# Optimization experiments

Measured on AMD Instinct MI355X. Metric: run time of the kernel, lower is better.

## Reference

```python
import jax, jax.numpy as jnp
import numpy as np

NUM_HEADS = 16
LN_EPS = 1e-5


def setup_inputs() -> dict:
    key = jax.random.key(0)
    ks = jax.random.split(key, 7)
    B, S, D = 4, 1024, 1024
    s_in = 1.0 / np.sqrt(D)
    return {
        "x": jax.random.normal(ks[0], (B, S, D), dtype=jnp.float32),
        # PyTorch MHA packed in-projection: [3D, D] weight, [3D] bias
        "w_qkv": jax.random.uniform(ks[1], (3 * D, D), dtype=jnp.float32, minval=-s_in, maxval=s_in),
        "b_qkv": jnp.zeros((3 * D,), dtype=jnp.float32),
        "w_out": jax.random.uniform(ks[2], (D, D), dtype=jnp.float32, minval=-s_in, maxval=s_in),
        "b_out": jnp.zeros((D,), dtype=jnp.float32),
        "ln_w": jnp.ones((D,), dtype=jnp.float32),
        "ln_b": jnp.zeros((D,), dtype=jnp.float32),
    }


def _layernorm(x, w, b):
    m = jnp.mean(x, axis=-1, keepdims=True)
    v = jnp.var(x, axis=-1, keepdims=True)
    return (x - m) * jax.lax.rsqrt(v + LN_EPS) * w + b


def reference(x, w_qkv, b_qkv, w_out, b_out, ln_w, ln_b):
    B, S, D = x.shape
    H = NUM_HEADS
    hd = D // H
    # packed QKV projection (torch: F.linear(x, w_qkv, b_qkv) then chunk)
    qkv = x @ w_qkv.T + b_qkv                      # [B, S, 3D]
    q, k, v = jnp.split(qkv, 3, axis=-1)
    q = q.reshape(B, S, H, hd).transpose(0, 2, 1, 3) * (hd ** -0.5)  # [B,H,S,hd]
    k = k.reshape(B, S, H, hd).transpose(0, 2, 1, 3)
    v = v.reshape(B, S, H, hd).transpose(0, 2, 1, 3)
    scores = jnp.einsum('bhqd,bhkd->bhqk', q, k)   # [B,H,S,S]
    attn = jax.nn.softmax(scores, axis=-1)
    ctx = jnp.einsum('bhqk,bhkd->bhqd', attn, v)   # [B,H,S,hd]
    ctx = ctx.transpose(0, 2, 1, 3).reshape(B, S, D)
    attn_out = ctx @ w_out.T + b_out
    # torch returns head-averaged weights (average_attn_weights=True)
    attn_weights = attn.mean(axis=1)               # [B,S,S]
    # dropout rate 0.0 -> identity; residual + LayerNorm
    y = _layernorm(x + attn_out, ln_w, ln_b)
    return y, attn_weights
```

## Files before the change

### kernel.cpp

```cpp
#include <hip/hip_runtime.h>
#include <cstdint>

typedef __bf16 bf16;
typedef __bf16 bf16x8 __attribute__((ext_vector_type(8)));
typedef __bf16 bf16x4 __attribute__((ext_vector_type(4)));
typedef float  f32x4  __attribute__((ext_vector_type(4)));

#define MFMA_BF16(a, b, c) __builtin_amdgcn_mfma_f32_16x16x32_bf16(a, b, c, 0, 0, 0)

#define WAITCNT_VM(n) asm volatile("s_waitcnt vmcnt(" #n ")" ::: "memory")
#define CFENCE()      asm volatile("" ::: "memory")

__device__ __forceinline__ void async_load16(const void* g, void* l) {
    __builtin_amdgcn_global_load_lds(
        (__attribute__((address_space(1))) uint32_t*)(uintptr_t)g,
        (__attribute__((address_space(3))) uint32_t*)(uint32_t)(uintptr_t)l,
        16, 0, 0);
}

__global__ void cvt_kernel(const float* __restrict__ src, bf16* __restrict__ dst, int n4) {
    int i = blockIdx.x * blockDim.x + threadIdx.x;
    if (i < n4) {
        float4 v = ((const float4*)src)[i];
        bf16x4 o;
        o[0] = (bf16)v.x; o[1] = (bf16)v.y; o[2] = (bf16)v.z; o[3] = (bf16)v.w;
        ((bf16x4*)dst)[i] = o;
    }
}

__global__ __launch_bounds__(256) void gemm_qkv_kernel(
    const bf16* __restrict__ A, const bf16* __restrict__ W,
    const float* __restrict__ bias,
    bf16* __restrict__ Qb, bf16* __restrict__ Kb, bf16* __restrict__ Vt)
{
    const int Kd = 1024;
    __shared__ bf16 sA[3][128 * 32];
    __shared__ bf16 sB[3][128 * 32];
    int tid = threadIdx.x, lane = tid & 63, wid = tid >> 6;
    int flat = blockIdx.y * 24 + blockIdx.x;
    int orig = (flat & 7) * 96 + (flat >> 3);
    int m0 = (orig / 24) * 128, n0 = (orig % 24) * 128;
    int srow = wid * 32 + (lane >> 2);
    int pchunk = lane & 3;
    int jchunk = pchunk ^ ((lane >> 3) & 3);
    const bf16* Ag = A + (size_t)(m0 + srow) * Kd + jchunk * 8;
    const bf16* Wg = W + (size_t)(n0 + srow) * Kd + jchunk * 8;
    int soff = srow * 32 + pchunk * 8;
    int wm = (wid & 1) * 64, wn = (wid >> 1) * 64;
    int lcol = lane & 15, quad = lane >> 4;
    int ckey = (lcol >> 1) & 3;
    f32x4 acc[4][4] = {};
#define STG_Q(buf, k0_) do { \
        async_load16(Ag + (k0_), &sA[buf][soff]); \
        async_load16(Ag + (k0_) + 16 * Kd, &sA[buf][soff + 512]); \
        async_load16(Wg + (k0_), &sB[buf][soff]); \
        async_load16(Wg + (k0_) + 16 * Kd, &sB[buf][soff + 512]); \
    } while (0)
    STG_Q(0, 0);
    STG_Q(1, 32);
    STG_Q(2, 64);
    int cur = 0;
    for (int it = 0; it < 32; ++it) {
        if (it < 30)      { WAITCNT_VM(8); }
        else if (it == 30){ WAITCNT_VM(4); }
        else              { WAITCNT_VM(0); }
        __builtin_amdgcn_s_barrier();
        CFENCE();
        const bf16* cA = sA[cur];
        const bf16* cB = sB[cur];
        bf16x8 af[4], bfr[4];
#pragma unroll
        for (int i = 0; i < 4; i++)
            af[i] = *(const bf16x8*)&cA[(wm + i * 16 + lcol) * 32 + (quad ^ ckey) * 8];
#pragma unroll
        for (int i = 0; i < 4; i++)
            bfr[i] = *(const bf16x8*)&cB[(wn + i * 16 + lcol) * 32 + (quad ^ ckey) * 8];
#pragma unroll
        for (int i = 0; i < 4; i++)
#pragma unroll
            for (int j = 0; j < 4; j++)
                acc[i][j] = MFMA_BF16(af[i], bfr[j], acc[i][j]);
        CFENCE();
        __builtin_amdgcn_s_barrier();
        if (it + 3 < 32) STG_Q(cur, (it + 3) * 32);
        cur = (cur == 2) ? 0 : cur + 1;
    }
#undef STG_Q
#pragma unroll
    for (int j = 0; j < 4; j++) {
        int n = n0 + wn + j * 16 + lcol;
        float bv = bias[n];
        int part = n >> 10, d = n & 1023, h = d >> 6, dd = d & 63;
#pragma unroll
        for (int i = 0; i < 4; i++) {
            int mb = m0 + wm + i * 16 + quad * 4;
            int b = mb >> 10, s = mb & 1023;
            if (part == 2) {
                bf16x4 v4;
#pragma unroll
                for (int r = 0; r < 4; r++) v4[r] = (bf16)(acc[i][j][r] + bv);
                *(bf16x4*)&Vt[(size_t)((b * 16 + h) * 64 + dd) * 1024 + s] = v4;
            } else {
                float scv = (part == 0) ? 0.125f : 1.0f;
                bf16* dst = (part == 0 ? Qb : Kb) + (size_t)((b * 16 + h) * 1024 + s) * 64 + dd;
#pragma unroll
                for (int r = 0; r < 4; r++) dst[(size_t)r * 64] = (bf16)((acc[i][j][r] + bv) * scv);
            }
        }
    }
}

__global__ __launch_bounds__(256) void gemm_out_kernel(
    const bf16* __restrict__ A, const bf16* __restrict__ W,
    const float* __restrict__ bias, float* __restrict__ out)
{
    const int Kd = 1024;
    __shared__ bf16 sA[3][64 * 32];
    __shared__ bf16 sB[3][128 * 32];
    int tid = threadIdx.x, lane = tid & 63, wid = tid >> 6;
    int m0 = blockIdx.y * 64, n0 = blockIdx.x * 128;
    int ra = tid >> 2;
    int pchunk = tid & 3;
    int jchunk = pchunk ^ ((tid >> 3) & 3);
    const bf16* Ag = A + (size_t)(m0 + ra) * Kd + jchunk * 8;
    const bf16* Wg = W + (size_t)(n0 + ra) * Kd + jchunk * 8;
    int aoff = ra * 32 + pchunk * 8;
    int wm = (wid & 1) * 32, wn = (wid >> 1) * 64;
    int lcol = lane & 15, quad = lane >> 4;
    int ckey = (lcol >> 1) & 3;
    f32x4 acc[2][4] = {};
#define STG_O(buf, k0_) do { \
        async_load16(Ag + (k0_), &sA[buf][aoff]); \
        async_load16(Wg + (k0_), &sB[buf][aoff]); \
        async_load16(Wg + (k0_) + 64 * Kd, &sB[buf][aoff + 64 * 32]); \
    } while (0)
    STG_O(0, 0);
    STG_O(1, 32);
    STG_O(2, 64);
    int cur = 0;
    for (int it = 0; it < 32; ++it) {
        if (it < 30)      { WAITCNT_VM(6); }
        else if (it == 30){ WAITCNT_VM(3); }
        else              { WAITCNT_VM(0); }
        __builtin_amdgcn_s_barrier();
        CFENCE();
        const bf16* cA = sA[cur];
        const bf16* cB = sB[cur];
        bf16x8 af[2], bfr[4];
#pragma unroll
        for (int i = 0; i < 2; i++)
            af[i] = *(const bf16x8*)&cA[(wm + i * 16 + lcol) * 32 + (quad ^ ckey) * 8];
#pragma unroll
        for (int j = 0; j < 4; j++)
            bfr[j] = *(const bf16x8*)&cB[(wn + j * 16 + lcol) * 32 + (quad ^ ckey) * 8];
#pragma unroll
        for (int i = 0; i < 2; i++)
#pragma unroll
            for (int j = 0; j < 4; j++)
                acc[i][j] = MFMA_BF16(af[i], bfr[j], acc[i][j]);
        CFENCE();
        __builtin_amdgcn_s_barrier();
        if (it + 3 < 32) STG_O(cur, (it + 3) * 32);
        cur = (cur == 2) ? 0 : cur + 1;
    }
#undef STG_O
#pragma unroll
    for (int j = 0; j < 4; j++) {
        int n = n0 + wn + j * 16 + lcol;
        float bv = bias[n];
#pragma unroll
        for (int i = 0; i < 2; i++) {
            int m = m0 + wm + i * 16 + quad * 4;
#pragma unroll
            for (int r = 0; r < 4; r++) out[(size_t)(m + r) * 1024 + n] = acc[i][j][r] + bv;
        }
    }
}

__global__ __launch_bounds__(512) void flash_kernel(
    const bf16* __restrict__ Qb, const bf16* __restrict__ Kb, const bf16* __restrict__ Vt,
    bf16* __restrict__ ctx, float* __restrict__ ml)
{
    __shared__ bf16 sK[2][64 * 64];
    __shared__ bf16 sV[2][64 * 64];
    __shared__ bf16 pt[8][16 * 64];
    int tid = threadIdx.x, lane = tid & 63, wid = tid >> 6;
    int bx = blockIdx.x;
    int orig = (bx & 7) * 64 + (bx >> 3);
    int qt = orig & 7;
    int h = (orig >> 3) & 15;
    int b = orig >> 7;
    int lcol = lane & 15, quad = lane >> 4;
    size_t base = (size_t)(b * 16 + h) * 65536;

    int q0 = qt * 128 + wid * 16;
    const bf16* qp = Qb + base + (size_t)(q0 + lcol) * 64 + quad * 8;
    bf16x8 a0 = *(const bf16x8*)qp;
    bf16x8 a1 = *(const bf16x8*)(qp + 32);

    char* wpt = (char*)&pt[wid][0];
    int sr = tid >> 3;
    int pp = tid & 7;
    int jj = pp ^ (sr & 7);
    int sw = lcol & 7;

#define STAGE_KV(buf, kt_) do { \
        async_load16(Kb + base + (size_t)((kt_) * 64 + sr) * 64 + jj * 8, &sK[buf][sr * 64 + pp * 8]); \
        async_load16(Vt + base + (size_t)sr * 1024 + (kt_) * 64 + jj * 8, &sV[buf][sr * 64 + pp * 8]); \
    } while (0)

    float l_[4] = {0.f, 0.f, 0.f, 0.f};
    f32x4 o[4] = {};

    STAGE_KV(0, 0);
    int cur = 0;
    for (int kt = 0; kt < 16; kt++) {
        __syncthreads();
        if (kt < 15) STAGE_KV(cur ^ 1, kt + 1);
        const bf16* sKc = &sK[cur][0];
        const bf16* sVc = &sV[cur][0];
#pragma unroll
        for (int nt = 0; nt < 4; nt++) {
            int ck = quad ^ sw;
            bf16x8 bk0 = *(const bf16x8*)&sKc[(nt * 16 + lcol) * 64 + ck * 8];
            bf16x8 bk1 = *(const bf16x8*)&sKc[(nt * 16 + lcol) * 64 + (ck ^ 4) * 8];
            f32x4 s = {};
            s = MFMA_BF16(a0, bk0, s);
            s = MFMA_BF16(a1, bk1, s);
#pragma unroll
            for (int rr = 0; rr < 4; rr++) {
                float p = __expf(s[rr]);
                l_[rr] += p;
                int row = quad * 4 + rr;
                *(bf16*)(wpt + row * 128 + ((nt * 32 + lcol * 2) ^ ((row & 7) << 4))) = (bf16)p;
            }
        }
#pragma unroll
        for (int kf = 0; kf < 2; kf++) {
            bf16x8 pa = *(const bf16x8*)(wpt + lcol * 128 + (((kf * 4 + quad) ^ sw) << 4));
#pragma unroll
            for (int dt = 0; dt < 4; dt++) {
                bf16x8 vb = *(const bf16x8*)&sVc[(dt * 16 + lcol) * 64 + ((kf * 4 + quad) ^ sw) * 8];
                o[dt] = MFMA_BF16(pa, vb, o[dt]);
            }
        }
        cur ^= 1;
    }
#undef STAGE_KV
#pragma unroll
    for (int mk = 1; mk < 16; mk <<= 1)
#pragma unroll
        for (int rr = 0; rr < 4; rr++) l_[rr] += __shfl_xor(l_[rr], mk, 64);
#pragma unroll
    for (int rr = 0; rr < 4; rr++) {
        float inv = 1.f / l_[rr];
        int qg = q0 + quad * 4 + rr;
#pragma unroll
        for (int dt = 0; dt < 4; dt++)
            ctx[(size_t)(b * 1024 + qg) * 1024 + h * 64 + dt * 16 + lcol] = (bf16)(o[dt][rr] * inv);
        if (lcol == 0)
            ml[(size_t)(b * 16 + h) * 1024 + qg] = l_[rr];
    }
}

__global__ __launch_bounds__(512) void aw_kernel(
    const bf16* __restrict__ Qb, const bf16* __restrict__ Kb,
    const float* __restrict__ ml, float* __restrict__ aw)
{
    __shared__ bf16 sK[2][64 * 64];
    int tid = threadIdx.x, lane = tid & 63, wid = tid >> 6;
    int bx = blockIdx.x;
    int orig = (bx & 7) * 64 + (bx >> 3);
    int kt = orig & 15;
    int qt = (orig >> 4) & 7;
    int b = orig >> 7;
    int lcol = lane & 15, quad = lane >> 4;
    int q0 = qt * 128 + wid * 16;
    int kbase = kt * 64;
    int sw = lcol & 7;
    int sr = tid >> 3, pp = tid & 7, jj = pp ^ (sr & 7);

#define STAGE_K(buf, hh) \
        async_load16(Kb + (size_t)(b * 16 + (hh)) * 65536 + (size_t)(kbase + sr) * 64 + jj * 8, \
                     &sK[buf][sr * 64 + pp * 8])

    float acc[16];
#pragma unroll
    for (int i = 0; i < 16; i++) acc[i] = 0.f;

    bf16x8 a0c, a1c, a0n, a1n;
    float4 mvC, mvN;
    {
        const bf16* qp = Qb + (size_t)(b * 16) * 65536 + (size_t)(q0 + lcol) * 64 + quad * 8;
        a0c = *(const bf16x8*)qp;
        a1c = *(const bf16x8*)(qp + 32);
        mvC = *(const float4*)(ml + (size_t)(b * 16) * 1024 + q0 + quad * 4);
    }
    STAGE_K(0, 0);
    int cur = 0;
    for (int h = 0; h < 16; h++) {
        __syncthreads();
        if (h < 15) {
            STAGE_K(cur ^ 1, h + 1);
            const bf16* qp = Qb + (size_t)(b * 16 + h + 1) * 65536 + (size_t)(q0 + lcol) * 64 + quad * 8;
            a0n = *(const bf16x8*)qp;
            a1n = *(const bf16x8*)(qp + 32);
            mvN = *(const float4*)(ml + (size_t)(b * 16 + h + 1) * 1024 + q0 + quad * 4);
        }
        float scale[4] = {0.0625f / mvC.x, 0.0625f / mvC.y, 0.0625f / mvC.z, 0.0625f / mvC.w};
#pragma unroll
        for (int nt = 0; nt < 4; nt++) {
            int ck = quad ^ sw;
            bf16x8 bk0 = *(const bf16x8*)&sK[cur][(nt * 16 + lcol) * 64 + ck * 8];
            bf16x8 bk1 = *(const bf16x8*)&sK[cur][(nt * 16 + lcol) * 64 + (ck ^ 4) * 8];
            f32x4 s = {};
            s = MFMA_BF16(a0c, bk0, s);
            s = MFMA_BF16(a1c, bk1, s);
#pragma unroll
            for (int rr = 0; rr < 4; rr++)
                acc[nt * 4 + rr] += __expf(s[rr]) * scale[rr];
        }
        if (h < 15) { a0c = a0n; a1c = a1n; mvC = mvN; }
        cur ^= 1;
    }
#undef STAGE_K
#pragma unroll
    for (int nt = 0; nt < 4; nt++)
#pragma unroll
        for (int rr = 0; rr < 4; rr++)
            aw[(size_t)(b * 1024 + q0 + quad * 4 + rr) * 1024 + kbase + nt * 16 + lcol] = acc[nt * 4 + rr];
}

__global__ __launch_bounds__(256) void ln_kernel(
    const float* __restrict__ x, const float* __restrict__ ao,
    const float* __restrict__ w, const float* __restrict__ bsh,
    float* __restrict__ y)
{
    int row = blockIdx.x, tid = threadIdx.x;
    float4 xv = ((const float4*)(x + (size_t)row * 1024))[tid];
    float4 av = ((const float4*)(ao + (size_t)row * 1024))[tid];
    float4 v = {xv.x + av.x, xv.y + av.y, xv.z + av.z, xv.w + av.w};
    float s = v.x + v.y + v.z + v.w;
    float ss = v.x * v.x + v.y * v.y + v.z * v.z + v.w * v.w;
#pragma unroll
    for (int off = 32; off; off >>= 1) { s += __shfl_down(s, off); ss += __shfl_down(ss, off); }
    __shared__ float rs[4], rss[4];
    int lane = tid & 63, wid = tid >> 6;
    if (lane == 0) { rs[wid] = s; rss[wid] = ss; }
    __syncthreads();
    s = rs[0] + rs[1] + rs[2] + rs[3];
    ss = rss[0] + rss[1] + rss[2] + rss[3];
    float mean = s * (1.f / 1024.f);
    float var = ss * (1.f / 1024.f) - mean * mean;
    float inv = rsqrtf(var + 1e-5f);
    float4 wv = ((const float4*)w)[tid];
    float4 bv = ((const float4*)bsh)[tid];
    float4 o;
    o.x = (v.x - mean) * inv * wv.x + bv.x;
    o.y = (v.y - mean) * inv * wv.y + bv.y;
    o.z = (v.z - mean) * inv * wv.z + bv.z;
    o.w = (v.w - mean) * inv * wv.w + bv.w;
    ((float4*)y)[row * 256 + tid] = o;
}

extern "C" void kernel_launch(void* const* d_in, const int* in_sizes, int n_in,
                              void* d_out, int out_size, void* d_ws, size_t ws_size,
                              hipStream_t stream) {
    const float* x     = (const float*)d_in[0];
    const float* w_qkv = (const float*)d_in[1];
    const float* b_qkv = (const float*)d_in[2];
    const float* w_out = (const float*)d_in[3];
    const float* b_out = (const float*)d_in[4];
    const float* ln_w  = (const float*)d_in[5];
    const float* ln_b  = (const float*)d_in[6];

    char* ws = (char*)d_ws;
    bf16*   Qb    = (bf16*)(ws);
    bf16*   Kb    = (bf16*)(ws + (8ull  << 20));
    bf16*   Vt    = (bf16*)(ws + (16ull << 20));
    bf16*   ctx   = (bf16*)(ws + (24ull << 20));
    float*  ml    = (float*)(ws + (32ull << 20));
    bf16*   x_bf  = (bf16*)(ws + (33ull << 20));
    bf16*   wq_bf = (bf16*)(ws + (41ull << 20));
    bf16*   wo_bf = (bf16*)(ws + (16ull << 20));
    float*  ao    = (float*)(ws);

    float* y_out  = (float*)d_out;
    float* aw_out = y_out + 4ull * 1024 * 1024;

    cvt_kernel<<<4096, 256, 0, stream>>>(x, x_bf, 1048576);
    cvt_kernel<<<3072, 256, 0, stream>>>(w_qkv, wq_bf, 786432);
    gemm_qkv_kernel<<<dim3(24, 32), 256, 0, stream>>>(x_bf, wq_bf, b_qkv, Qb, Kb, Vt);
    flash_kernel<<<512, 512, 0, stream>>>(Qb, Kb, Vt, ctx, ml);
    aw_kernel<<<512, 512, 0, stream>>>(Qb, Kb, ml, aw_out);
    cvt_kernel<<<1024, 256, 0, stream>>>(w_out, wo_bf, 262144);
    gemm_out_kernel<<<dim3(8, 64), 256, 0, stream>>>(ctx, wo_bf, b_out, ao);
    ln_kernel<<<4096, 256, 0, stream>>>(x, ao, ln_w, ln_b, y_out);
}
```

Before: 208.9 us.

## Stage GEMM and attention epilogues through LDS and merge conversion launches

The QKV GEMM epilogue now writes each output tile into shared memory and then emits coalesced 16-byte stores to Q, K and the transposed V, replacing scattered 2-byte and 8-byte global stores. The flash kernel likewise stages its context output through its per-warp LDS scratch so it can write 16-byte vectors. The two input conversion kernels become one launch, and the w_out conversion is folded into extra blocks of the attention-weights kernel. This cuts uncoalesced store traffic and launch count, at the cost of extra LDS traffic and a barrier in the epilogues.

```diff
diff --git a/kernel.cpp b/kernel.cpp
--- a/kernel.cpp
+++ b/kernel.cpp
@@ -18,14 +18,16 @@
         16, 0, 0);
 }
 
-__global__ void cvt_kernel(const float* __restrict__ src, bf16* __restrict__ dst, int n4) {
+__global__ void cvt3_kernel(const float* __restrict__ s0, bf16* __restrict__ d0, int n0,
+                            const float* __restrict__ s1, bf16* __restrict__ d1, int n1) {
     int i = blockIdx.x * blockDim.x + threadIdx.x;
-    if (i < n4) {
-        float4 v = ((const float4*)src)[i];
-        bf16x4 o;
-        o[0] = (bf16)v.x; o[1] = (bf16)v.y; o[2] = (bf16)v.z; o[3] = (bf16)v.w;
-        ((bf16x4*)dst)[i] = o;
-    }
+    const float* s; bf16* d; int j = i;
+    if (j < n0) { s = s0; d = d0; }
+    else { j -= n0; if (j >= n1) return; s = s1; d = d1; }
+    float4 v = ((const float4*)s)[j];
+    bf16x4 o;
+    o[0] = (bf16)v.x; o[1] = (bf16)v.y; o[2] = (bf16)v.z; o[3] = (bf16)v.w;
+    ((bf16x4*)d)[j] = o;
 }
 
 __global__ __launch_bounds__(256) void gemm_qkv_kernel(
@@ -34,8 +36,9 @@
     bf16* __restrict__ Qb, bf16* __restrict__ Kb, bf16* __restrict__ Vt)
 {
     const int Kd = 1024;
-    __shared__ bf16 sA[3][128 * 32];
-    __shared__ bf16 sB[3][128 * 32];
+    __shared__ __attribute__((aligned(16))) bf16 smem[6 * 128 * 32];
+    bf16* const sA0 = smem;
+    bf16* const sB0 = smem + 3 * 4096;
     int tid = threadIdx.x, lane = tid & 63, wid = tid >> 6;
     int flat = blockIdx.y * 24 + blockIdx.x;
     int orig = (flat & 7) * 96 + (flat >> 3);
@@ -51,10 +54,10 @@
     int ckey = (lcol >> 1) & 3;
     f32x4 acc[4][4] = {};
 #define STG_Q(buf, k0_) do { \
-        async_load16(Ag + (k0_), &sA[buf][soff]); \
-        async_load16(Ag + (k0_) + 16 * Kd, &sA[buf][soff + 512]); \
-        async_load16(Wg + (k0_), &sB[buf][soff]); \
-        async_load16(Wg + (k0_) + 16 * Kd, &sB[buf][soff + 512]); \
+        async_load16(Ag + (k0_), sA0 + (buf) * 4096 + soff); \
+        async_load16(Ag + (k0_) + 16 * Kd, sA0 + (buf) * 4096 + soff + 512); \
+        async_load16(Wg + (k0_), sB0 + (buf) * 4096 + soff); \
+        async_load16(Wg + (k0_) + 16 * Kd, sB0 + (buf) * 4096 + soff + 512); \
     } while (0)
     STG_Q(0, 0);
     STG_Q(1, 32);
@@ -66,8 +69,8 @@
         else              { WAITCNT_VM(0); }
         __builtin_amdgcn_s_barrier();
         CFENCE();
-        const bf16* cA = sA[cur];
-        const bf16* cB = sB[cur];
+        const bf16* cA = sA0 + cur * 4096;
+        const bf16* cB = sB0 + cur * 4096;
         bf16x8 af[4], bfr[4];
 #pragma unroll
         for (int i = 0; i < 4; i++)
@@ -86,26 +89,49 @@
         cur = (cur == 2) ? 0 : cur + 1;
     }
 #undef STG_Q
-#pragma unroll
-    for (int j = 0; j < 4; j++) {
-        int n = n0 + wn + j * 16 + lcol;
-        float bv = bias[n];
-        int part = n >> 10, d = n & 1023, h = d >> 6, dd = d & 63;
-#pragma unroll
-        for (int i = 0; i < 4; i++) {
-            int mb = m0 + wm + i * 16 + quad * 4;
-            int b = mb >> 10, s = mb & 1023;
-            if (part == 2) {
-                bf16x4 v4;
-#pragma unroll
-                for (int r = 0; r < 4; r++) v4[r] = (bf16)(acc[i][j][r] + bv);
-                *(bf16x4*)&Vt[(size_t)((b * 16 + h) * 64 + dd) * 1024 + s] = v4;
-            } else {
-                float scv = (part == 0) ? 0.125f : 1.0f;
-                bf16* dst = (part == 0 ? Qb : Kb) + (size_t)((b * 16 + h) * 1024 + s) * 64 + dd;
-#pragma unroll
-                for (int r = 0; r < 4; r++) dst[(size_t)r * 64] = (bf16)((acc[i][j][r] + bv) * scv);
-            }
+    const int LP = 136;
+    bf16* sE = smem;
+    int part = n0 >> 10;
+    int h0 = (n0 & 1023) >> 6;
+    int b = m0 >> 10, s0 = m0 & 1023;
+    if (part == 2) {
+#pragma unroll
+        for (int j = 0; j < 4; j++) {
+            float bv = bias[n0 + wn + j * 16 + lcol];
+#pragma unroll
+            for (int i = 0; i < 4; i++)
+#pragma unroll
+                for (int r = 0; r < 4; r++)
+                    sE[(wn + j * 16 + lcol) * LP + (wm + i * 16 + quad * 4 + r)] = (bf16)(acc[i][j][r] + bv);
+        }
+        __syncthreads();
+#pragma unroll
+        for (int p = 0; p < 8; p++) {
+            int c = p * 256 + tid;
+            int nl = c >> 4, mc = (c & 15) * 8;
+            int dd = nl & 63, h = h0 + (nl >> 6);
+            *(bf16x8*)&Vt[(size_t)((b * 16 + h) * 64 + dd) * 1024 + s0 + mc] = *(const bf16x8*)&sE[nl * LP + mc];
+        }
+    } else {
+        float scv = (part == 0) ? 0.125f : 1.0f;
+        bf16* dst = (part == 0) ? Qb : Kb;
+#pragma unroll
+        for (int j = 0; j < 4; j++) {
+            float bv = bias[n0 + wn + j * 16 + lcol];
+#pragma unroll
+            for (int i = 0; i < 4; i++)
+#pragma unroll
+                for (int r = 0; r < 4; r++)
+                    sE[(wm + i * 16 + quad * 4 + r) * LP + (wn + j * 16 + lcol)] = (bf16)((acc[i][j][r] + bv) * scv);
+        }
+        __syncthreads();
+#pragma unroll
+        for (int p = 0; p < 8; p++) {
+            int c = p * 256 + tid;
+            int half = c >> 10, idx = c & 1023;
+            int m = idx >> 3, nc = (idx & 7) * 8;
+            *(bf16x8*)&dst[(size_t)((b * 16 + h0 + half) * 1024 + s0 + m) * 64 + nc] =
+                *(const bf16x8*)&sE[m * LP + half * 64 + nc];
         }
     }
 }
@@ -254,22 +280,38 @@
 #pragma unroll
     for (int rr = 0; rr < 4; rr++) {
         float inv = 1.f / l_[rr];
-        int qg = q0 + quad * 4 + rr;
+        int row = quad * 4 + rr;
 #pragma unroll
         for (int dt = 0; dt < 4; dt++)
-            ctx[(size_t)(b * 1024 + qg) * 1024 + h * 64 + dt * 16 + lcol] = (bf16)(o[dt][rr] * inv);
+            *(bf16*)(wpt + row * 128 + ((dt * 32 + lcol * 2) ^ ((row & 7) << 4))) = (bf16)(o[dt][rr] * inv);
         if (lcol == 0)
-            ml[(size_t)(b * 16 + h) * 1024 + qg] = l_[rr];
+            ml[(size_t)(b * 16 + h) * 1024 + q0 + row] = l_[rr];
+    }
+    int r8a = lane >> 3, ca = lane & 7;
+#pragma unroll
+    for (int half = 0; half < 2; half++) {
+        int r8 = r8a + half * 8;
+        bf16x8 v = *(const bf16x8*)(wpt + r8 * 128 + ((ca * 16) ^ ((r8 & 7) << 4)));
+        *(bf16x8*)&ctx[(size_t)(b * 1024 + q0 + r8) * 1024 + h * 64 + ca * 8] = v;
     }
 }
 
 __global__ __launch_bounds__(512) void aw_kernel(
     const bf16* __restrict__ Qb, const bf16* __restrict__ Kb,
-    const float* __restrict__ ml, float* __restrict__ aw)
+    const float* __restrict__ ml, float* __restrict__ aw,
+    const float* __restrict__ wof, bf16* __restrict__ wob)
 {
     __shared__ bf16 sK[2][64 * 64];
     int tid = threadIdx.x, lane = tid & 63, wid = tid >> 6;
     int bx = blockIdx.x;
+    if (bx >= 512) {
+        int i = (bx - 512) * 512 + tid;
+        float4 v = ((const float4*)wof)[i];
+        bf16x4 o;
+        o[0] = (bf16)v.x; o[1] = (bf16)v.y; o[2] = (bf16)v.z; o[3] = (bf16)v.w;
+        ((bf16x4*)wob)[i] = o;
+        return;
+    }
     int orig = (bx & 7) * 64 + (bx >> 3);
     int kt = orig & 15;
     int qt = (orig >> 4) & 7;
@@ -388,12 +430,10 @@
     float* y_out  = (float*)d_out;
     float* aw_out = y_out + 4ull * 1024 * 1024;
 
-    cvt_kernel<<<4096, 256, 0, stream>>>(x, x_bf, 1048576);
-    cvt_kernel<<<3072, 256, 0, stream>>>(w_qkv, wq_bf, 786432);
+    cvt3_kernel<<<7168, 256, 0, stream>>>(x, x_bf, 1048576, w_qkv, wq_bf, 786432);
     gemm_qkv_kernel<<<dim3(24, 32), 256, 0, stream>>>(x_bf, wq_bf, b_qkv, Qb, Kb, Vt);
     flash_kernel<<<512, 512, 0, stream>>>(Qb, Kb, Vt, ctx, ml);
-    aw_kernel<<<512, 512, 0, stream>>>(Qb, Kb, ml, aw_out);
-    cvt_kernel<<<1024, 256, 0, stream>>>(w_out, wo_bf, 262144);
+    aw_kernel<<<1024, 512, 0, stream>>>(Qb, Kb, ml, aw_out, w_out, wo_bf);
     gemm_out_kernel<<<dim3(8, 64), 256, 0, stream>>>(ctx, wo_bf, b_out, ao);
     ln_kernel<<<4096, 256, 0, stream>>>(x, ao, ln_w, ln_b, y_out);
 }
```

Measured after the change: 201.2 us. 1.04x faster.
